# Performance work log

Hardware: AMD Instinct MI355X
Metric: run time of the kernel (lower is better)

The kernel has to match this reference:

```python
import jax, jax.numpy as jnp
import numpy as np

KERNEL_SIZE = 7  # matches init_kwargs


def setup_inputs() -> dict:
    key = jax.random.key(0)
    k1, k2 = jax.random.split(key)
    x = jax.random.normal(k1, (32, 512, 4096), dtype=jnp.float32)
    # nn.Parameter(torch.rand(1, 1, 2k-1)) -> uniform [0,1)
    kernel_total = jax.random.uniform(k2, (1, 1, 2 * KERNEL_SIZE - 1), dtype=jnp.float32)
    return {"x": x, "kernel_total": kernel_total}


def reference(x, kernel_total):
    # Original math (after the rolled copies / stack / cat / mul-sum dance):
    #   out[b,c,l] = sum_{i=0}^{k-1} w[i] * x[b,c,l-i]      (zero-padded left)
    #             + sum_{i=1}^{k-1} w[k-1+i] * x[b,c,l+i]   (zero-padded right)
    # i.e. a depthwise 1D cross-correlation with an asymmetric 2k-1 tap kernel
    # shared across all channels. We express it as a single fused conv instead of
    # materializing 2k-1 rolled copies.
    k = KERNEL_SIZE
    w = kernel_total.reshape(-1)  # (2k-1,)
    # Cross-correlation kernel over offsets d = -(k-1)..(k-1):
    #   d <= 0 -> w[-d]  (the "previous" taps), d > 0 -> w[k-1+d] (the "behind" taps)
    kern = jnp.concatenate([w[:k][::-1], w[k:]])  # (2k-1,)
    B, C, L = x.shape
    xr = x.reshape(B * C, 1, L)  # fold channels into batch: same kernel per channel
    out = jax.lax.conv_general_dilated(
        xr,
        kern.reshape(1, 1, 2 * k - 1),
        window_strides=(1,),
        padding=[(k - 1, k - 1)],
        dimension_numbers=("NCH", "OIH", "NCH"),
    )
    return out.reshape(B, C, L)
```

## Files before the change

### kernel.cpp

```cpp
#include <hip/hip_runtime.h>


#define ROW_L 4096
#define KHALF 7
#define TAPS 13
#define HALO 6

__global__ __launch_bounds__(256) void conv13_rows_kernel(
    const float* __restrict__ x,
    const float* __restrict__ w,
    float* __restrict__ out)
{
    __shared__ __align__(16) float s[ROW_L + 2 * HALO + 4];

    const int row = blockIdx.x;
    const int tid = threadIdx.x;
    const float* xr = x + (size_t)row * ROW_L;
    float* outr = out + (size_t)row * ROW_L;

    float c[TAPS];
#pragma unroll
    for (int t = 0; t < TAPS; ++t)
        c[t] = (t <= HALO) ? w[HALO - t] : w[t];

    if (tid < HALO) {
        s[tid] = 0.0f;
        s[ROW_L + HALO + tid] = 0.0f;
    }

#pragma unroll
    for (int i = 0; i < 4; ++i) {
        const int j4 = tid + i * 256;
        float4 v = ((const float4*)xr)[j4];
        const int base = HALO + j4 * 4;
        s[base + 0] = v.x;
        s[base + 1] = v.y;
        s[base + 2] = v.z;
        s[base + 3] = v.w;
    }
    __syncthreads();

#pragma unroll
    for (int i = 0; i < 4; ++i) {
        const int j4 = tid + i * 256;
        const int j = j4 * 4;

        const float4 a0 = *(const float4*)&s[j + 0];
        const float4 a1 = *(const float4*)&s[j + 4];
        const float4 a2 = *(const float4*)&s[j + 8];
        const float4 a3 = *(const float4*)&s[j + 12];
        const float r[16] = {a0.x, a0.y, a0.z, a0.w,
                             a1.x, a1.y, a1.z, a1.w,
                             a2.x, a2.y, a2.z, a2.w,
                             a3.x, a3.y, a3.z, a3.w};

        float acc0 = 0.f, acc1 = 0.f, acc2 = 0.f, acc3 = 0.f;
#pragma unroll
        for (int t = 0; t < TAPS; ++t) {
            acc0 = fmaf(c[t], r[t + 0], acc0);
            acc1 = fmaf(c[t], r[t + 1], acc1);
            acc2 = fmaf(c[t], r[t + 2], acc2);
            acc3 = fmaf(c[t], r[t + 3], acc3);
        }

        float4 o;
        o.x = acc0; o.y = acc1; o.z = acc2; o.w = acc3;
        ((float4*)outr)[j4] = o;
    }
}

extern "C" void kernel_launch(void* const* d_in, const int* in_sizes, int n_in,
                              void* d_out, int out_size, void* d_ws, size_t ws_size,
                              hipStream_t stream) {
    const float* x = (const float*)d_in[0];
    const float* w = (const float*)d_in[1];
    float* out = (float*)d_out;

    const int rows = in_sizes[0] / ROW_L;
    conv13_rows_kernel<<<rows, 256, 0, stream>>>(x, w, out);
}
```

Baseline: 429.1 us.

## Replace shared-memory staging with direct register loads of 16-element chunks plus halo

Each thread now loads its contiguous 16-element chunk and neighbouring halo float4s straight from global memory into registers and computes 16 outputs, removing the LDS staging and the block barrier. Halo loads are served mostly by cache, but each thread's accesses are strided by 64 bytes, so per-instruction coalescing is worse than the previous interleaved float4 pattern. Register pressure also rises.

```diff
diff --git a/kernel.cpp b/kernel.cpp
--- a/kernel.cpp
+++ b/kernel.cpp
@@ -2,70 +2,64 @@
 
 
 #define ROW_L 4096
-#define KHALF 7
 #define TAPS 13
 #define HALO 6
+#define CHUNKS_PER_ROW 256
 
-__global__ __launch_bounds__(256) void conv13_rows_kernel(
+__global__ __launch_bounds__(256) void conv13_direct_kernel(
     const float* __restrict__ x,
     const float* __restrict__ w,
     float* __restrict__ out)
 {
-    __shared__ __align__(16) float s[ROW_L + 2 * HALO + 4];
-
     const int row = blockIdx.x;
-    const int tid = threadIdx.x;
-    const float* xr = x + (size_t)row * ROW_L;
-    float* outr = out + (size_t)row * ROW_L;
+    const int chunk = threadIdx.x;
+    const size_t base = (size_t)row * ROW_L + (size_t)chunk * 16;
+    const float4* x4 = (const float4*)(x + base);
+    float4* o4 = (float4*)(out + base);
 
     float c[TAPS];
 #pragma unroll
     for (int t = 0; t < TAPS; ++t)
         c[t] = (t <= HALO) ? w[HALO - t] : w[t];
 
-    if (tid < HALO) {
-        s[tid] = 0.0f;
-        s[ROW_L + HALO + tid] = 0.0f;
+    const float4 z4 = make_float4(0.f, 0.f, 0.f, 0.f);
+    float4 rm2 = z4, rm1 = z4, rp4 = z4, rp5 = z4;
+    if (chunk > 0)                   { rm2 = x4[-2]; rm1 = x4[-1]; }
+    if (chunk < CHUNKS_PER_ROW - 1)  { rp4 = x4[4];  rp5 = x4[5]; }
+    const float4 r0 = x4[0];
+    const float4 r1 = x4[1];
+    const float4 r2 = x4[2];
+    const float4 r3 = x4[3];
+
+    const float in[28] = {
+        rm2.z, rm2.w,
+        rm1.x, rm1.y, rm1.z, rm1.w,
+        r0.x, r0.y, r0.z, r0.w,
+        r1.x, r1.y, r1.z, r1.w,
+        r2.x, r2.y, r2.z, r2.w,
+        r3.x, r3.y, r3.z, r3.w,
+        rp4.x, rp4.y, rp4.z, rp4.w,
+        rp5.x, rp5.y
+    };
+
+    float acc[16];
+#pragma unroll
+    for (int i = 0; i < 16; ++i) {
+        float a = 0.f;
+#pragma unroll
+        for (int t = 0; t < TAPS; ++t)
+            a = fmaf(c[t], in[i + t], a);
+        acc[i] = a;
     }
 
 #pragma unroll
-    for (int i = 0; i < 4; ++i) {
-        const int j4 = tid + i * 256;
-        float4 v = ((const float4*)xr)[j4];
-        const int base = HALO + j4 * 4;
-        s[base + 0] = v.x;
-        s[base + 1] = v.y;
-        s[base + 2] = v.z;
-        s[base + 3] = v.w;
-    }
-    __syncthreads();
-
-#pragma unroll
-    for (int i = 0; i < 4; ++i) {
-        const int j4 = tid + i * 256;
-        const int j = j4 * 4;
-
-        const float4 a0 = *(const float4*)&s[j + 0];
-        const float4 a1 = *(const float4*)&s[j + 4];
-        const float4 a2 = *(const float4*)&s[j + 8];
-        const float4 a3 = *(const float4*)&s[j + 12];
-        const float r[16] = {a0.x, a0.y, a0.z, a0.w,
-                             a1.x, a1.y, a1.z, a1.w,
-                             a2.x, a2.y, a2.z, a2.w,
-                             a3.x, a3.y, a3.z, a3.w};
-
-        float acc0 = 0.f, acc1 = 0.f, acc2 = 0.f, acc3 = 0.f;
-#pragma unroll
-        for (int t = 0; t < TAPS; ++t) {
-            acc0 = fmaf(c[t], r[t + 0], acc0);
-            acc1 = fmaf(c[t], r[t + 1], acc1);
-            acc2 = fmaf(c[t], r[t + 2], acc2);
-            acc3 = fmaf(c[t], r[t + 3], acc3);
-        }
-
+    for (int g = 0; g < 4; ++g) {
         float4 o;
-        o.x = acc0; o.y = acc1; o.z = acc2; o.w = acc3;
-        ((float4*)outr)[j4] = o;
+        o.x = acc[g * 4 + 0];
+        o.y = acc[g * 4 + 1];
+        o.z = acc[g * 4 + 2];
+        o.w = acc[g * 4 + 3];
+        o4[g] = o;
     }
 }
 
@@ -77,5 +71,5 @@
     float* out = (float*)d_out;
 
     const int rows = in_sizes[0] / ROW_L;
-    conv13_rows_kernel<<<rows, 256, 0, stream>>>(x, w, out);
+    conv13_direct_kernel<<<rows, 256, 0, stream>>>(x, w, out);
 }
```

Result: slower. 466.3 us (+8.7%).
